# Optimization experiments

Measured on AMD Instinct MI355X. Metric: run time of the kernel, lower is better.

The kernel has to match this reference:

```python
import jax, jax.numpy as jnp
import numpy as np

A = 81          # agents / zones (9x9 grid)
DMAX = 5        # max neighborhood size (self + 4-neighbors)
NGLOB = 48      # global obs block width
HID = 128
B = 16384
LN_EPS = 1e-12  # tf.contrib.layers.layer_norm epsilon
BN_EPS = 1e-3   # tf.contrib.layers.batch_norm epsilon
NEG = -1e30


def _grid_adjacency():
    side = 9
    idx = np.zeros((A, DMAX), np.int32)
    mask = np.zeros((A, DMAX), bool)
    for i in range(A):
        r, c = divmod(i, side)
        nb = [i]
        for dr, dc in ((-1, 0), (1, 0), (0, -1), (0, 1)):
            rr, cc = r + dr, c + dc
            if 0 <= rr < side and 0 <= cc < side:
                nb.append(rr * side + cc)
        idx[i, :len(nb)] = nb
        mask[i, :len(nb)] = True
    return jnp.asarray(idx), jnp.asarray(mask)


def setup_inputs() -> dict:
    key = jax.random.key(0)
    ks = jax.random.split(key, 8)
    neigh_idx, neigh_mask = _grid_adjacency()
    in_dim = 2 * DMAX + NGLOB  # padded local obs width (58)
    s = 0.05
    return {
        "obs": jax.random.normal(ks[0], (B, 210), jnp.float32),
        "neigh_idx": neigh_idx,
        "neigh_mask": neigh_mask,
        "W1": jax.random.normal(ks[1], (A, in_dim, HID), jnp.float32) * s,
        "b1": jnp.zeros((A, HID), jnp.float32),
        "ln1_g": jnp.ones((A, HID), jnp.float32),
        "ln1_b": jnp.zeros((A, HID), jnp.float32),
        "bn1_b": jnp.zeros((A, HID), jnp.float32),
        "W2": jax.random.normal(ks[2], (A, HID, HID), jnp.float32) * s,
        "b2": jnp.zeros((A, HID), jnp.float32),
        "ln2_g": jnp.ones((A, HID), jnp.float32),
        "ln2_b": jnp.zeros((A, HID), jnp.float32),
        "bn2_b": jnp.zeros((A, HID), jnp.float32),
        "Wout": jax.random.normal(ks[3], (A, HID, DMAX), jnp.float32) * s,
        "bout": jnp.zeros((A, DMAX), jnp.float32),
    }


def _layer_norm(x, g, b):
    mu = jnp.mean(x, axis=-1, keepdims=True)
    var = jnp.mean(jnp.square(x - mu), axis=-1, keepdims=True)
    return (x - mu) * jax.lax.rsqrt(var + LN_EPS) * g[:, None, :] + b[:, None, :]


def _batch_norm(x, beta):
    # training-mode batch norm over the batch axis (axis=1), center only (scale=False)
    mu = jnp.mean(x, axis=1, keepdims=True)
    var = jnp.mean(jnp.square(x - mu), axis=1, keepdims=True)
    return (x - mu) * jax.lax.rsqrt(var + BN_EPS) + beta[:, None, :]


def reference(obs, neigh_idx, neigh_mask, W1, b1, ln1_g, ln1_b, bn1_b,
              W2, b2, ln2_g, ln2_b, bn2_b, Wout, bout):
    m = neigh_mask[:, None, :].astype(obs.dtype)          # [A,1,DMAX]
    g1 = obs[:, NGLOB + neigh_idx].transpose(1, 0, 2)      # [A,B,DMAX] zone block 1
    g2 = obs[:, NGLOB + 81 + neigh_idx].transpose(1, 0, 2)  # [A,B,DMAX] zone block 2
    glob = jnp.broadcast_to(obs[None, :, :NGLOB], (A, obs.shape[0], NGLOB))
    x = jnp.concatenate([g1 * m, g2 * m, glob], axis=-1)   # [A,B,58] (padded slots zeroed)

    h = jnp.einsum('abi,aio->abo', x, W1) + b1[:, None, :]
    h = jax.nn.relu(_batch_norm(_layer_norm(h, ln1_g, ln1_b), bn1_b))
    h = jnp.einsum('abi,aio->abo', h, W2) + b2[:, None, :]
    h = jax.nn.relu(_batch_norm(_layer_norm(h, ln2_g, ln2_b), bn2_b))

    logits = jnp.einsum('abi,aid->abd', h, Wout) + bout[:, None, :]  # [A,B,DMAX]
    logits = jnp.where(neigh_mask[:, None, :], logits, NEG)
    p = jax.nn.softmax(logits, axis=-1) * m                # masked softmax over valid neighbors

    oh = jax.nn.one_hot(neigh_idx, A, dtype=p.dtype)       # [A,DMAX,81] scatter map
    out = jnp.einsum('abd,adn->abn', p, oh)                # scatter into fixed 81-vector
    return out.transpose(1, 0, 2)                          # [B,A,81]
```

## Files before the change

### kernel.cpp

```cpp
#include <hip/hip_runtime.h>
#include <stdint.h>
#include <stddef.h>

#define N_AG 81

typedef __bf16 bf16x8 __attribute__((ext_vector_type(8)));
typedef float f32x4 __attribute__((ext_vector_type(4)));
typedef uint32_t u32v4 __attribute__((ext_vector_type(4)));
typedef uint32_t u32v2 __attribute__((ext_vector_type(2)));

#define PB 0
#define PG 128
#define PBT 256

#define SWZ(row, off) ((uint32_t)(off) ^ (((uint32_t)(row) & 7u) << 4))

__device__ __forceinline__ unsigned short b2u(__bf16 h) {
  return __builtin_bit_cast(unsigned short, h);
}

__device__ __forceinline__ f32x4 f4z() { f32x4 v; v[0]=0.f; v[1]=0.f; v[2]=0.f; v[3]=0.f; return v; }

__device__ __forceinline__ bf16x8 ld_frag(const uint8_t* p) {
  u32v4 v = *(const u32v4*)p;
  return __builtin_bit_cast(bf16x8, v);
}

__device__ __forceinline__ f32x4 mfma16(bf16x8 a, bf16x8 b, f32x4 c) {
  return __builtin_amdgcn_mfma_f32_16x16x32_bf16(a, b, c, 0, 0, 0);
}

__device__ __forceinline__ uint8_t* yslot(float* out, int b, int a) {
  size_t base = (size_t)b * 26244 + (size_t)a * 324;
  uint32_t pad = (uint32_t)(64 - (base & 63)) & 63u;
  return (uint8_t*)out + base + pad;
}

__device__ __forceinline__ float wave16_sum(float v) {
  v += __builtin_bit_cast(float, __builtin_amdgcn_update_dpp(0, __builtin_bit_cast(int, v), 0xB1, 0xF, 0xF, true));
  v += __builtin_bit_cast(float, __builtin_amdgcn_update_dpp(0, __builtin_bit_cast(int, v), 0x4E, 0xF, 0xF, true));
  v += __builtin_bit_cast(float, __builtin_amdgcn_update_dpp(0, __builtin_bit_cast(int, v), 0x141, 0xF, 0xF, true));
  v += __builtin_bit_cast(float, __builtin_amdgcn_update_dpp(0, __builtin_bit_cast(int, v), 0x140, 0xF, 0xF, true));
  return v;
}

__device__ __forceinline__ bf16x8 mk_frag(const unsigned short (&us)[8]) {
  u32v4 pk;
  pk[0] = (uint32_t)us[0] | ((uint32_t)us[1] << 16);
  pk[1] = (uint32_t)us[2] | ((uint32_t)us[3] << 16);
  pk[2] = (uint32_t)us[4] | ((uint32_t)us[5] << 16);
  pk[3] = (uint32_t)us[6] | ((uint32_t)us[7] << 16);
  return __builtin_bit_cast(bf16x8, pk);
}

__device__ __forceinline__ bf16x8 bn_frag(u32v4 yv, const f32x4 (&cf)[4]) {
  bf16x8 r;
  #pragma unroll
  for (int j = 0; j < 8; ++j) {
    uint32_t us = (j & 1) ? (yv[j >> 1] >> 16) : (yv[j >> 1] & 0xffffu);
    float f = __builtin_bit_cast(float, us << 16);
    float h = fmaf(f, cf[j >> 1][(j & 1) * 2], cf[j >> 1][(j & 1) * 2 + 1]);
    r[j] = (__bf16)fmaxf(h, 0.f);
  }
  return r;
}

__device__ __forceinline__ void bias_ln(f32x4 (&acc)[8][2], const float* s_par, int g) {
  #pragma unroll
  for (int nf = 0; nf < 2; ++nf) {
    float s = 0.f, qs = 0.f;
    #pragma unroll
    for (int mf = 0; mf < 8; ++mf) {
      #pragma unroll
      for (int rg = 0; rg < 4; ++rg) {
        float tv = acc[mf][nf][rg] + s_par[PB + 16 * mf + 4 * g + rg];
        acc[mf][nf][rg] = tv;
        s += tv;
        qs = fmaf(tv, tv, qs);
      }
    }
    s += __shfl_xor(s, 16);  s += __shfl_xor(s, 32);
    qs += __shfl_xor(qs, 16); qs += __shfl_xor(qs, 32);
    float mu = s * (1.f / 128.f);
    float var = qs * (1.f / 128.f) - mu * mu;
    float rstd = rsqrtf(var + 1e-12f);
    #pragma unroll
    for (int mf = 0; mf < 8; ++mf) {
      #pragma unroll
      for (int rg = 0; rg < 4; ++rg) {
        int o = 16 * mf + 4 * g + rg;
        acc[mf][nf][rg] = (acc[mf][nf][rg] - mu) * rstd * s_par[PG + o] + s_par[PBT + o];
      }
    }
  }
}

__device__ __forceinline__ void stats_lds(const f32x4 (&acc)[8][2],
                                          float (&s_red)[2][4][128],
                                          int wv, int g, int q) {
  #pragma unroll
  for (int mf = 0; mf < 8; ++mf) {
    #pragma unroll
    for (int rg = 0; rg < 4; ++rg) {
      float a0v = acc[mf][0][rg], a1v = acc[mf][1][rg];
      float s = a0v + a1v;
      float qq = fmaf(a0v, a0v, a1v * a1v);
      s = wave16_sum(s);
      qq = wave16_sum(qq);
      if (q == 0) {
        int o = 16 * mf + 4 * g + rg;
        s_red[0][wv][o] += s;
        s_red[1][wv][o] += qq;
      }
    }
  }
}

__device__ __forceinline__ void pack_lds(const f32x4 (&acc)[8][2], uint8_t* s_y,
                                         int wv, int g, int q) {
  #pragma unroll
  for (int nf = 0; nf < 2; ++nf) {
    uint32_t row = 32 * wv + 16 * nf + q;
    #pragma unroll
    for (int mf = 0; mf < 8; ++mf) {
      u32v2 pk;
      pk[0] = (uint32_t)b2u((__bf16)acc[mf][nf][0]) | ((uint32_t)b2u((__bf16)acc[mf][nf][1]) << 16);
      pk[1] = (uint32_t)b2u((__bf16)acc[mf][nf][2]) | ((uint32_t)b2u((__bf16)acc[mf][nf][3]) << 16);
      *(u32v2*)(s_y + row * 256 + SWZ(row, 32 * mf + 8 * g)) = pk;
    }
  }
}

__device__ __forceinline__ void burst_out(const uint8_t* s_y, float* out, int tile, int a, int t) {
  const int row = t >> 1, half = t & 1;
  uint8_t* sp = yslot(out, tile * 128 + row, a) + half * 128;
  #pragma unroll
  for (int j = 0; j < 8; ++j) {
    u32v4 v = *(const u32v4*)(s_y + row * 256 + SWZ(row, half * 128 + 16 * j));
    *(u32v4*)(sp + 16 * j) = v;
  }
}

__device__ __forceinline__ void burst_in(uint8_t* s_y, float* out, int tile, int a, int t) {
  const int row = t >> 1, half = t & 1;
  const uint8_t* sp = yslot(out, tile * 128 + row, a) + half * 128;
  #pragma unroll
  for (int j = 0; j < 8; ++j) {
    u32v4 v = *(const u32v4*)(sp + 16 * j);
    *(u32v4*)(s_y + row * 256 + SWZ(row, half * 128 + 16 * j)) = v;
  }
}

__global__ void prep_w1(const float* __restrict__ W1, uint8_t* __restrict__ w1img) {
  const int a = blockIdx.x, t = threadIdx.x;
  for (int i = t; i < 128 * 64; i += 256) {
    int o = i & 127, kk = i >> 7;
    float v;
    if (kk < 48)      v = W1[((size_t)a * 58 + (10 + kk)) * 128 + o];
    else if (kk < 58) v = W1[((size_t)a * 58 + (kk - 48)) * 128 + o];
    else              v = 0.f;
    uint32_t cb = 2u * kk;
    uint32_t phys = o * 128 + (((cb & ~15u) ^ (((uint32_t)o & 7u) << 4)) | (cb & 15u));
    *(unsigned short*)(w1img + (size_t)a * 16384 + phys) = b2u((__bf16)v);
  }
}

__global__ void prep_w2wo(const float* __restrict__ W2, const float* __restrict__ Wout,
                          uint8_t* __restrict__ w2img, uint8_t* __restrict__ woimg) {
  const int a = blockIdx.x, t = threadIdx.x;
  for (int i = t; i < 128 * 128; i += 256) {
    int o = i & 127, kk = i >> 7;
    float v = W2[((size_t)a * 128 + kk) * 128 + o];
    uint32_t cb = 2u * kk;
    uint32_t phys = o * 256 + (((cb & ~15u) ^ (((uint32_t)o & 7u) << 4)) | (cb & 15u));
    *(unsigned short*)(w2img + (size_t)a * 32768 + phys) = b2u((__bf16)v);
  }
  for (int i = t; i < 16 * 128; i += 256) {
    int k = i & 127, d = i >> 7;
    float v = (d < 5) ? Wout[((size_t)a * 128 + k) * 5 + d] : 0.f;
    uint32_t cb = 2u * k;
    uint32_t phys = d * 256 + (((cb & ~15u) ^ (((uint32_t)d & 7u) << 4)) | (cb & 15u));
    *(unsigned short*)(woimg + (size_t)a * 4096 + phys) = b2u((__bf16)v);
  }
}

__global__ void prep_obs(const float* __restrict__ obs, uint8_t* __restrict__ globimg) {
  const int row = blockIdx.x * 256 + threadIdx.x;
  if (row >= 16384) return;
  const float* orow = obs + (size_t)row * 210;
  uint8_t* dst = globimg + (size_t)row * 96;
  #pragma unroll
  for (int c = 0; c < 6; ++c) {
    u32v4 pk;
    #pragma unroll
    for (int e = 0; e < 4; ++e) {
      pk[e] = (uint32_t)b2u((__bf16)orow[8 * c + 2 * e]) |
              ((uint32_t)b2u((__bf16)orow[8 * c + 2 * e + 1]) << 16);
    }
    *(u32v4*)(dst + 16 * c) = pk;
  }
}

__global__ void prep_zimgT(const float* __restrict__ obs, unsigned short* __restrict__ zimgT) {
  __shared__ unsigned short lt[128][164];
  const int t = threadIdx.x;
  const int b0 = blockIdx.x * 128;
  for (int i = t; i < 128 * 162; i += 256) {
    int br = i / 162, n = i - 162 * br;
    lt[br][n] = b2u((__bf16)obs[(size_t)(b0 + br) * 210 + 48 + n]);
  }
  __syncthreads();
  for (int i = t; i < 162 * 128; i += 256) {
    int n = i >> 7, br = i & 127;
    zimgT[(size_t)n * 16384 + b0 + br] = lt[br][n];
  }
}

__global__ void reduce_bn(const float* __restrict__ S, const float* __restrict__ Q,
                          const float* __restrict__ beta, float2* __restrict__ bn) {
  const int a = blockIdx.x, k = threadIdx.x;
  float mu = S[a * 128 + k] * (1.f / 16384.f);
  float var = Q[a * 128 + k] * (1.f / 16384.f) - mu * mu;
  float rs = rsqrtf(var + 1e-3f);
  bn[a * 128 + k] = make_float2(rs, beta[a * 128 + k] - mu * rs);
}

__launch_bounds__(256, 2)
__global__ void pass1_kernel(const int* __restrict__ nidx,
                             const float* __restrict__ b1, const float* __restrict__ ln1g,
                             const float* __restrict__ ln1b,
                             const uint8_t* __restrict__ w1img,
                             const uint8_t* __restrict__ globimg,
                             const unsigned short* __restrict__ zimgT,
                             float* __restrict__ statS, float* __restrict__ statQ,
                             float* __restrict__ out) {
  __shared__ __align__(16) uint8_t s_w1[16384];
  __shared__ __align__(16) uint8_t s_y[32768];
  __shared__ float s_par[384];
  __shared__ float s_red[2][4][128];

  const int t = threadIdx.x;
  const int wv = t >> 6, l = t & 63, g = l >> 4, q = l & 15;
  const int a = blockIdx.x >> 5;
  const int sub = blockIdx.x & 31;

  const int r9 = a / 9, c9 = a - 9 * r9;
  const int deg = 1 + (r9 > 0) + (r9 < 8) + (c9 > 0) + (c9 < 8);
  int nid[5];
  #pragma unroll
  for (int d = 0; d < 5; ++d) nid[d] = __builtin_amdgcn_readfirstlane(nidx[a * 5 + d]);

  const uint8_t* w1src = w1img + (size_t)a * 16384;
  #pragma unroll
  for (int i = 0; i < 4; ++i) ((u32v4*)s_w1)[t + 256 * i] = ((const u32v4*)w1src)[t + 256 * i];
  if (t < 128) {
    s_par[PB + t] = b1[a * 128 + t];
    s_par[PG + t] = ln1g[a * 128 + t];
    s_par[PBT + t] = ln1b[a * 128 + t];
  }
  #pragma unroll
  for (int i = 0; i < 4; ++i) ((float*)s_red)[t + 256 * i] = 0.f;
  __syncthreads();

  for (int tt = 0; tt < 4; ++tt) {
    const int tile = sub * 4 + tt;

    bf16x8 bfr[2][2];
    #pragma unroll
    for (int ks = 0; ks < 2; ++ks) {
      #pragma unroll
      for (int nf = 0; nf < 2; ++nf) {
        const int brow = tile * 128 + 32 * wv + 16 * nf + q;
        if (ks == 1 && g >= 2) {
          unsigned short us[8];
          if (g == 2) {
            #pragma unroll
            for (int e = 0; e < 5; ++e)
              us[e] = (e < deg) ? zimgT[(size_t)nid[e] * 16384 + brow] : (unsigned short)0;
            #pragma unroll
            for (int e = 0; e < 3; ++e)
              us[5 + e] = (e < deg) ? zimgT[(size_t)(81 + nid[e]) * 16384 + brow] : (unsigned short)0;
          } else {
            us[0] = (3 < deg) ? zimgT[(size_t)(81 + nid[3]) * 16384 + brow] : (unsigned short)0;
            us[1] = (4 < deg) ? zimgT[(size_t)(81 + nid[4]) * 16384 + brow] : (unsigned short)0;
            #pragma unroll
            for (int e = 2; e < 8; ++e) us[e] = 0;
          }
          bfr[ks][nf] = mk_frag(us);
        } else {
          bfr[ks][nf] = *(const bf16x8*)(globimg + (size_t)brow * 96 + (32 * ks + 8 * g) * 2);
        }
      }
    }

    f32x4 acc[8][2];
    #pragma unroll
    for (int mf = 0; mf < 8; ++mf) { acc[mf][0] = f4z(); acc[mf][1] = f4z(); }
    #pragma unroll
    for (int ks = 0; ks < 2; ++ks) {
      #pragma unroll
      for (int mf = 0; mf < 8; ++mf) {
        uint32_t r = 16 * mf + q;
        uint32_t cb = ((uint32_t)(64 * ks + 16 * g)) ^ ((r & 7u) << 4);
        bf16x8 af = ld_frag(s_w1 + r * 128 + cb);
        acc[mf][0] = mfma16(af, bfr[ks][0], acc[mf][0]);
        acc[mf][1] = mfma16(af, bfr[ks][1], acc[mf][1]);
      }
    }

    bias_ln(acc, s_par, g);
    stats_lds(acc, s_red, wv, g, q);
    pack_lds(acc, s_y, wv, g, q);
    __syncthreads();
    burst_out(s_y, out, tile, a, t);
    __syncthreads();
  }

  if (t < 128) {
    float S = s_red[0][0][t] + s_red[0][1][t] + s_red[0][2][t] + s_red[0][3][t];
    float Q = s_red[1][0][t] + s_red[1][1][t] + s_red[1][2][t] + s_red[1][3][t];
    atomicAdd(statS + a * 128 + t, S);
    atomicAdd(statQ + a * 128 + t, Q);
  }
}

__launch_bounds__(256, 2)
__global__ void pass2_kernel(const float* __restrict__ b2, const float* __restrict__ ln2g,
                             const float* __restrict__ ln2b,
                             const uint8_t* __restrict__ w2img,
                             const float2* __restrict__ bn1,
                             float* __restrict__ statS, float* __restrict__ statQ,
                             float* __restrict__ out) {
  __shared__ __align__(16) uint8_t s_w2[32768];
  __shared__ __align__(16) uint8_t s_y[32768];
  __shared__ float s_par[384];
  __shared__ __align__(16) float2 s_bnc[128];
  __shared__ float s_red[2][4][128];

  const int t = threadIdx.x;
  const int wv = t >> 6, l = t & 63, g = l >> 4, q = l & 15;
  const int a = blockIdx.x >> 5;
  const int sub = blockIdx.x & 31;

  const uint8_t* w2src = w2img + (size_t)a * 32768;
  #pragma unroll
  for (int i = 0; i < 8; ++i) ((u32v4*)s_w2)[t + 256 * i] = ((const u32v4*)w2src)[t + 256 * i];
  if (t < 128) {
    s_par[PB + t] = b2[a * 128 + t];
    s_par[PG + t] = ln2g[a * 128 + t];
    s_par[PBT + t] = ln2b[a * 128 + t];
    s_bnc[t] = bn1[a * 128 + t];
  }
  #pragma unroll
  for (int i = 0; i < 4; ++i) ((float*)s_red)[t + 256 * i] = 0.f;
  __syncthreads();

  for (int tt = 0; tt < 4; ++tt) {
    const int tile = sub * 4 + tt;

    burst_in(s_y, out, tile, a, t);
    __syncthreads();

    f32x4 acc[8][2];
    #pragma unroll
    for (int mf = 0; mf < 8; ++mf) { acc[mf][0] = f4z(); acc[mf][1] = f4z(); }

    #pragma unroll
    for (int ks2 = 0; ks2 < 4; ++ks2) {
      const int k0 = 32 * ks2 + 8 * g;
      f32x4 cf[4];
      #pragma unroll
      for (int i = 0; i < 4; ++i)
        cf[i] = *(const f32x4*)((const uint8_t*)s_bnc + k0 * 8 + 16 * i);
      bf16x8 bfr[2];
      #pragma unroll
      for (int nf = 0; nf < 2; ++nf) {
        uint32_t row = 32 * wv + 16 * nf + q;
        u32v4 yv = *(const u32v4*)(s_y + row * 256 + SWZ(row, 64 * ks2 + 16 * g));
        bfr[nf] = bn_frag(yv, cf);
      }
      #pragma unroll
      for (int mf = 0; mf < 8; ++mf) {
        uint32_t r = 16 * mf + q;
        uint32_t cb = ((uint32_t)(64 * ks2 + 16 * g)) ^ ((r & 7u) << 4);
        bf16x8 af = ld_frag(s_w2 + r * 256 + cb);
        acc[mf][0] = mfma16(af, bfr[0], acc[mf][0]);
        acc[mf][1] = mfma16(af, bfr[1], acc[mf][1]);
      }
    }

    bias_ln(acc, s_par, g);
    stats_lds(acc, s_red, wv, g, q);
    __syncthreads();
    pack_lds(acc, s_y, wv, g, q);
    __syncthreads();
    burst_out(s_y, out, tile, a, t);
    __syncthreads();
  }

  if (t < 128) {
    float S = s_red[0][0][t] + s_red[0][1][t] + s_red[0][2][t] + s_red[0][3][t];
    float Q = s_red[1][0][t] + s_red[1][1][t] + s_red[1][2][t] + s_red[1][3][t];
    atomicAdd(statS + a * 128 + t, S);
    atomicAdd(statQ + a * 128 + t, Q);
  }
}

__launch_bounds__(256, 3)
__global__ void pass3_kernel(const int* __restrict__ nidx, const float* __restrict__ boutp,
                             const uint8_t* __restrict__ woimg,
                             const float2* __restrict__ bn2,
                             float* __restrict__ out) {
  __shared__ __align__(16) uint8_t s_buf[43008];
  __shared__ __align__(16) uint8_t s_wo[4096];
  __shared__ __align__(16) float2 s_bnc[128];
  __shared__ float s_bout[16];

  uint8_t* s_y = s_buf;
  float* s_out = (float*)s_buf;

  const int t = threadIdx.x;
  const int wv = t >> 6, l = t & 63, g = l >> 4, q = l & 15;
  const int a = blockIdx.x >> 5;
  const int sub = blockIdx.x & 31;

  const int r9 = a / 9, c9 = a - 9 * r9;
  const int deg = 1 + (r9 > 0) + (r9 < 8) + (c9 > 0) + (c9 < 8);
  int nid[5];
  #pragma unroll
  for (int d = 0; d < 5; ++d) nid[d] = __builtin_amdgcn_readfirstlane(nidx[a * 5 + d]);

  ((u32v4*)s_wo)[t] = ((const u32v4*)(woimg + (size_t)a * 4096))[t];
  if (t < 128) s_bnc[t] = bn2[a * 128 + t];
  if (t < 16) s_bout[t] = (t < 5) ? boutp[a * 5 + t] : 0.f;
  __syncthreads();

  bf16x8 afr[4];
  #pragma unroll
  for (int ks2 = 0; ks2 < 4; ++ks2) {
    uint32_t cb = ((uint32_t)(64 * ks2 + 16 * g)) ^ (((uint32_t)q & 7u) << 4);
    afr[ks2] = ld_frag(s_wo + q * 256 + cb);
  }

  for (int tt = 0; tt < 4; ++tt) {
    const int tile = sub * 4 + tt;

    burst_in(s_y, out, tile, a, t);
    __syncthreads();

    f32x4 accd[2];
    accd[0] = f4z(); accd[1] = f4z();

    #pragma unroll
    for (int ks2 = 0; ks2 < 4; ++ks2) {
      const int k0 = 32 * ks2 + 8 * g;
      f32x4 cf[4];
      #pragma unroll
      for (int i = 0; i < 4; ++i)
        cf[i] = *(const f32x4*)((const uint8_t*)s_bnc + k0 * 8 + 16 * i);
      #pragma unroll
      for (int nf = 0; nf < 2; ++nf) {
        uint32_t row = 32 * wv + 16 * nf + q;
        u32v4 yv = *(const u32v4*)(s_y + row * 256 + SWZ(row, 64 * ks2 + 16 * g));
        accd[nf] = mfma16(afr[ks2], bn_frag(yv, cf), accd[nf]);
      }
    }

    #pragma unroll
    for (int nf = 0; nf < 2; ++nf) {
      #pragma unroll
      for (int rg = 0; rg < 4; ++rg) accd[nf][rg] += s_bout[4 * g + rg];
    }
    float d4[2];
    d4[0] = __shfl_xor(accd[0][0], 16);
    d4[1] = __shfl_xor(accd[1][0], 16);

    float p[2][5];
    #pragma unroll
    for (int nf = 0; nf < 2; ++nf) {
      float v[5] = {accd[nf][0], accd[nf][1], accd[nf][2], accd[nf][3], d4[nf]};
      float mx = v[0];
      #pragma unroll
      for (int d = 1; d < 5; ++d)
        if (d < deg) mx = fmaxf(mx, v[d]);
      float den = 0.f;
      #pragma unroll
      for (int d = 0; d < 5; ++d) {
        float e = (d < deg) ? __expf(v[d] - mx) : 0.f;
        p[nf][d] = e;
        den += e;
      }
      float inv = 1.f / den;
      #pragma unroll
      for (int d = 0; d < 5; ++d) p[nf][d] *= inv;
    }

    float p5[5];
    #pragma unroll
    for (int d = 0; d < 5; ++d) {
      float pr = __shfl_xor(p[1][d], 32);
      p5[d] = (g == 0) ? p[0][d] : pr;
    }

    __syncthreads();
    #pragma unroll
    for (int i = 0; i < 11; ++i) {
      int idx = t + 256 * i;
      if (idx < 2688) {
        u32v4 z; z[0] = 0u; z[1] = 0u; z[2] = 0u; z[3] = 0u;
        ((u32v4*)s_out)[idx] = z;
      }
    }
    __syncthreads();
    if (g == 0 || g == 2) {
      const int row = 32 * wv + ((g == 2) ? 16 : 0) + q;
      #pragma unroll
      for (int d = 0; d < 5; ++d)
        if (d < deg) s_out[row * 84 + nid[d]] = p5[d];
    }
    __syncthreads();
    const size_t obase = (size_t)(tile * 128) * 6561 + (size_t)a * 81;
    for (int i = t; i < 128 * 81; i += 256) {
      int r = i / 81;
      int n = i - r * 81;
      out[obase + (size_t)r * 6561 + n] = s_out[r * 84 + n];
    }
    __syncthreads();
  }
}

extern "C" void kernel_launch(void* const* d_in, const int* in_sizes, int n_in,
                              void* d_out, int out_size, void* d_ws, size_t ws_size,
                              hipStream_t stream) {
  (void)in_sizes; (void)n_in; (void)out_size; (void)ws_size;
  const float* obs = (const float*)d_in[0];
  const int* nidx = (const int*)d_in[1];
  const float* W1 = (const float*)d_in[3];
  const float* b1 = (const float*)d_in[4];
  const float* ln1g = (const float*)d_in[5];
  const float* ln1b = (const float*)d_in[6];
  const float* bnb1 = (const float*)d_in[7];
  const float* W2 = (const float*)d_in[8];
  const float* b2 = (const float*)d_in[9];
  const float* ln2g = (const float*)d_in[10];
  const float* ln2b = (const float*)d_in[11];
  const float* bnb2 = (const float*)d_in[12];
  const float* Wout = (const float*)d_in[13];
  const float* bout = (const float*)d_in[14];
  float* out = (float*)d_out;
  uint8_t* ws = (uint8_t*)d_ws;

  uint8_t* w1img   = ws;
  uint8_t* globimg = ws + 1327104;
  uint8_t* regionA = ws + 2899968;
  unsigned short* zimgT = (unsigned short*)regionA;
  uint8_t* w2img = regionA;
  uint8_t* woimg = regionA + 2654208;
  float* statS = (float*)(ws + 8208384);
  float* statQ = (float*)(ws + 8249856);
  float2* bn1 = (float2*)(ws + 8291328);
  float2* bn2 = (float2*)(ws + 8374272);

  prep_w1<<<N_AG, 256, 0, stream>>>(W1, w1img);
  prep_obs<<<64, 256, 0, stream>>>(obs, globimg);
  prep_zimgT<<<128, 256, 0, stream>>>(obs, zimgT);
  hipMemsetAsync(statS, 0, 2 * 41472, stream);

  pass1_kernel<<<N_AG * 32, 256, 0, stream>>>(nidx, b1, ln1g, ln1b, w1img, globimg, zimgT,
                                              statS, statQ, out);
  reduce_bn<<<N_AG, 128, 0, stream>>>(statS, statQ, bnb1, bn1);

  prep_w2wo<<<N_AG, 256, 0, stream>>>(W2, Wout, w2img, woimg);
  hipMemsetAsync(statS, 0, 2 * 41472, stream);

  pass2_kernel<<<N_AG * 32, 256, 0, stream>>>(b2, ln2g, ln2b, w2img, bn1,
                                              statS, statQ, out);
  reduce_bn<<<N_AG, 128, 0, stream>>>(statS, statQ, bnb2, bn2);

  pass3_kernel<<<N_AG * 32, 256, 0, stream>>>(nidx, bout, woimg, bn2, out);
}
```

Before: 777.8 us.

## Use 512-thread blocks with one 16-row N-fragment per wave across passes

All three pass kernels move from 256 to 512 threads per block. Each of the 8 waves now owns 16 batch rows instead of 32, which halves the per-thread accumulator registers and lets more waves hide latency. Pass3 replaces the block-wide zero/scatter/copy of the output tile with per-wave bands, removing two block barriers per tile. reduce_bn now zeroes the stat buffers itself, which drops one memset launch, at the cost of less per-wave reuse of each loaded weight fragment.

New measurement: 958.0 us. +23.2%, slower.

```diff
diff --git a/kernel.cpp b/kernel.cpp
--- a/kernel.cpp
+++ b/kernel.cpp
@@ -65,46 +65,42 @@
   return r;
 }
 
-__device__ __forceinline__ void bias_ln(f32x4 (&acc)[8][2], const float* s_par, int g) {
-  #pragma unroll
-  for (int nf = 0; nf < 2; ++nf) {
-    float s = 0.f, qs = 0.f;
-    #pragma unroll
-    for (int mf = 0; mf < 8; ++mf) {
-      #pragma unroll
-      for (int rg = 0; rg < 4; ++rg) {
-        float tv = acc[mf][nf][rg] + s_par[PB + 16 * mf + 4 * g + rg];
-        acc[mf][nf][rg] = tv;
-        s += tv;
-        qs = fmaf(tv, tv, qs);
-      }
-    }
-    s += __shfl_xor(s, 16);  s += __shfl_xor(s, 32);
-    qs += __shfl_xor(qs, 16); qs += __shfl_xor(qs, 32);
-    float mu = s * (1.f / 128.f);
-    float var = qs * (1.f / 128.f) - mu * mu;
-    float rstd = rsqrtf(var + 1e-12f);
-    #pragma unroll
-    for (int mf = 0; mf < 8; ++mf) {
-      #pragma unroll
-      for (int rg = 0; rg < 4; ++rg) {
-        int o = 16 * mf + 4 * g + rg;
-        acc[mf][nf][rg] = (acc[mf][nf][rg] - mu) * rstd * s_par[PG + o] + s_par[PBT + o];
-      }
-    }
-  }
-}
-
-__device__ __forceinline__ void stats_lds(const f32x4 (&acc)[8][2],
-                                          float (&s_red)[2][4][128],
-                                          int wv, int g, int q) {
+__device__ __forceinline__ void bias_ln1(f32x4 (&acc)[8], const float* s_par, int g) {
+  float s = 0.f, qs = 0.f;
   #pragma unroll
   for (int mf = 0; mf < 8; ++mf) {
     #pragma unroll
     for (int rg = 0; rg < 4; ++rg) {
-      float a0v = acc[mf][0][rg], a1v = acc[mf][1][rg];
-      float s = a0v + a1v;
-      float qq = fmaf(a0v, a0v, a1v * a1v);
+      float tv = acc[mf][rg] + s_par[PB + 16 * mf + 4 * g + rg];
+      acc[mf][rg] = tv;
+      s += tv;
+      qs = fmaf(tv, tv, qs);
+    }
+  }
+  s += __shfl_xor(s, 16);  s += __shfl_xor(s, 32);
+  qs += __shfl_xor(qs, 16); qs += __shfl_xor(qs, 32);
+  float mu = s * (1.f / 128.f);
+  float var = qs * (1.f / 128.f) - mu * mu;
+  float rstd = rsqrtf(var + 1e-12f);
+  #pragma unroll
+  for (int mf = 0; mf < 8; ++mf) {
+    #pragma unroll
+    for (int rg = 0; rg < 4; ++rg) {
+      int o = 16 * mf + 4 * g + rg;
+      acc[mf][rg] = (acc[mf][rg] - mu) * rstd * s_par[PG + o] + s_par[PBT + o];
+    }
+  }
+}
+
+__device__ __forceinline__ void stats_lds1(const f32x4 (&acc)[8],
+                                           float (&s_red)[2][8][128],
+                                           int wv, int g, int q) {
+  #pragma unroll
+  for (int mf = 0; mf < 8; ++mf) {
+    #pragma unroll
+    for (int rg = 0; rg < 4; ++rg) {
+      float s = acc[mf][rg];
+      float qq = s * s;
       s = wave16_sum(s);
       qq = wave16_sum(qq);
       if (q == 0) {
@@ -116,38 +112,35 @@
   }
 }
 
-__device__ __forceinline__ void pack_lds(const f32x4 (&acc)[8][2], uint8_t* s_y,
-                                         int wv, int g, int q) {
-  #pragma unroll
-  for (int nf = 0; nf < 2; ++nf) {
-    uint32_t row = 32 * wv + 16 * nf + q;
-    #pragma unroll
-    for (int mf = 0; mf < 8; ++mf) {
-      u32v2 pk;
-      pk[0] = (uint32_t)b2u((__bf16)acc[mf][nf][0]) | ((uint32_t)b2u((__bf16)acc[mf][nf][1]) << 16);
-      pk[1] = (uint32_t)b2u((__bf16)acc[mf][nf][2]) | ((uint32_t)b2u((__bf16)acc[mf][nf][3]) << 16);
-      *(u32v2*)(s_y + row * 256 + SWZ(row, 32 * mf + 8 * g)) = pk;
-    }
-  }
-}
-
-__device__ __forceinline__ void burst_out(const uint8_t* s_y, float* out, int tile, int a, int t) {
-  const int row = t >> 1, half = t & 1;
-  uint8_t* sp = yslot(out, tile * 128 + row, a) + half * 128;
-  #pragma unroll
-  for (int j = 0; j < 8; ++j) {
-    u32v4 v = *(const u32v4*)(s_y + row * 256 + SWZ(row, half * 128 + 16 * j));
+__device__ __forceinline__ void pack_lds1(const f32x4 (&acc)[8], uint8_t* s_y,
+                                          int wv, int g, int q) {
+  uint32_t row = 16 * wv + q;
+  #pragma unroll
+  for (int mf = 0; mf < 8; ++mf) {
+    u32v2 pk;
+    pk[0] = (uint32_t)b2u((__bf16)acc[mf][0]) | ((uint32_t)b2u((__bf16)acc[mf][1]) << 16);
+    pk[1] = (uint32_t)b2u((__bf16)acc[mf][2]) | ((uint32_t)b2u((__bf16)acc[mf][3]) << 16);
+    *(u32v2*)(s_y + row * 256 + SWZ(row, 32 * mf + 8 * g)) = pk;
+  }
+}
+
+__device__ __forceinline__ void burst_out512(const uint8_t* s_y, float* out, int tile, int a, int t) {
+  const int row = t >> 2, qt = t & 3;
+  uint8_t* sp = yslot(out, tile * 128 + row, a) + qt * 64;
+  #pragma unroll
+  for (int j = 0; j < 4; ++j) {
+    u32v4 v = *(const u32v4*)(s_y + row * 256 + SWZ(row, qt * 64 + 16 * j));
     *(u32v4*)(sp + 16 * j) = v;
   }
 }
 
-__device__ __forceinline__ void burst_in(uint8_t* s_y, float* out, int tile, int a, int t) {
-  const int row = t >> 1, half = t & 1;
-  const uint8_t* sp = yslot(out, tile * 128 + row, a) + half * 128;
-  #pragma unroll
-  for (int j = 0; j < 8; ++j) {
+__device__ __forceinline__ void burst_in512(uint8_t* s_y, float* out, int tile, int a, int t) {
+  const int row = t >> 2, qt = t & 3;
+  const uint8_t* sp = yslot(out, tile * 128 + row, a) + qt * 64;
+  #pragma unroll
+  for (int j = 0; j < 4; ++j) {
     u32v4 v = *(const u32v4*)(sp + 16 * j);
-    *(u32v4*)(s_y + row * 256 + SWZ(row, half * 128 + 16 * j)) = v;
+    *(u32v4*)(s_y + row * 256 + SWZ(row, qt * 64 + 16 * j)) = v;
   }
 }
 
@@ -216,16 +209,18 @@
   }
 }
 
-__global__ void reduce_bn(const float* __restrict__ S, const float* __restrict__ Q,
+__global__ void reduce_bn(float* __restrict__ S, float* __restrict__ Q,
                           const float* __restrict__ beta, float2* __restrict__ bn) {
   const int a = blockIdx.x, k = threadIdx.x;
   float mu = S[a * 128 + k] * (1.f / 16384.f);
   float var = Q[a * 128 + k] * (1.f / 16384.f) - mu * mu;
   float rs = rsqrtf(var + 1e-3f);
   bn[a * 128 + k] = make_float2(rs, beta[a * 128 + k] - mu * rs);
-}
-
-__launch_bounds__(256, 2)
+  S[a * 128 + k] = 0.f;
+  Q[a * 128 + k] = 0.f;
+}
+
+__launch_bounds__(512, 4)
 __global__ void pass1_kernel(const int* __restrict__ nidx,
                              const float* __restrict__ b1, const float* __restrict__ ln1g,
                              const float* __restrict__ ln1b,
@@ -237,7 +232,7 @@
   __shared__ __align__(16) uint8_t s_w1[16384];
   __shared__ __align__(16) uint8_t s_y[32768];
   __shared__ float s_par[384];
-  __shared__ float s_red[2][4][128];
+  __shared__ float s_red[2][8][128];
 
   const int t = threadIdx.x;
   const int wv = t >> 6, l = t & 63, g = l >> 4, q = l & 15;
@@ -252,50 +247,47 @@
 
   const uint8_t* w1src = w1img + (size_t)a * 16384;
   #pragma unroll
-  for (int i = 0; i < 4; ++i) ((u32v4*)s_w1)[t + 256 * i] = ((const u32v4*)w1src)[t + 256 * i];
+  for (int i = 0; i < 2; ++i) ((u32v4*)s_w1)[t + 512 * i] = ((const u32v4*)w1src)[t + 512 * i];
   if (t < 128) {
     s_par[PB + t] = b1[a * 128 + t];
     s_par[PG + t] = ln1g[a * 128 + t];
     s_par[PBT + t] = ln1b[a * 128 + t];
   }
   #pragma unroll
-  for (int i = 0; i < 4; ++i) ((float*)s_red)[t + 256 * i] = 0.f;
+  for (int i = 0; i < 4; ++i) ((float*)s_red)[t + 512 * i] = 0.f;
   __syncthreads();
 
   for (int tt = 0; tt < 4; ++tt) {
     const int tile = sub * 4 + tt;
-
-    bf16x8 bfr[2][2];
+    const int brow = tile * 128 + 16 * wv + q;
+
+    bf16x8 bfr[2];
     #pragma unroll
     for (int ks = 0; ks < 2; ++ks) {
-      #pragma unroll
-      for (int nf = 0; nf < 2; ++nf) {
-        const int brow = tile * 128 + 32 * wv + 16 * nf + q;
-        if (ks == 1 && g >= 2) {
-          unsigned short us[8];
-          if (g == 2) {
-            #pragma unroll
-            for (int e = 0; e < 5; ++e)
-              us[e] = (e < deg) ? zimgT[(size_t)nid[e] * 16384 + brow] : (unsigned short)0;
-            #pragma unroll
-            for (int e = 0; e < 3; ++e)
-              us[5 + e] = (e < deg) ? zimgT[(size_t)(81 + nid[e]) * 16384 + brow] : (unsigned short)0;
-          } else {
-            us[0] = (3 < deg) ? zimgT[(size_t)(81 + nid[3]) * 16384 + brow] : (unsigned short)0;
-            us[1] = (4 < deg) ? zimgT[(size_t)(81 + nid[4]) * 16384 + brow] : (unsigned short)0;
-            #pragma unroll
-            for (int e = 2; e < 8; ++e) us[e] = 0;
-          }
-          bfr[ks][nf] = mk_frag(us);
+      if (ks == 1 && g >= 2) {
+        unsigned short us[8];
+        if (g == 2) {
+          #pragma unroll
+          for (int e = 0; e < 5; ++e)
+            us[e] = (e < deg) ? zimgT[(size_t)nid[e] * 16384 + brow] : (unsigned short)0;
+          #pragma unroll
+          for (int e = 0; e < 3; ++e)
+            us[5 + e] = (e < deg) ? zimgT[(size_t)(81 + nid[e]) * 16384 + brow] : (unsigned short)0;
         } else {
-          bfr[ks][nf] = *(const bf16x8*)(globimg + (size_t)brow * 96 + (32 * ks + 8 * g) * 2);
+          us[0] = (3 < deg) ? zimgT[(size_t)(81 + nid[3]) * 16384 + brow] : (unsigned short)0;
+          us[1] = (4 < deg) ? zimgT[(size_t)(81 + nid[4]) * 16384 + brow] : (unsigned short)0;
+          #pragma unroll
+          for (int e = 2; e < 8; ++e) us[e] = 0;
         }
-      }
-    }
-
-    f32x4 acc[8][2];
-    #pragma unroll
-    for (int mf = 0; mf < 8; ++mf) { acc[mf][0] = f4z(); acc[mf][1] = f4z(); }
+        bfr[ks] = mk_frag(us);
+      } else {
+        bfr[ks] = *(const bf16x8*)(globimg + (size_t)brow * 96 + (32 * ks + 8 * g) * 2);
+      }
+    }
+
+    f32x4 acc[8];
+    #pragma unroll
+    for (int mf = 0; mf < 8; ++mf) acc[mf] = f4z();
     #pragma unroll
     for (int ks = 0; ks < 2; ++ks) {
       #pragma unroll
@@ -303,28 +295,28 @@
         uint32_t r = 16 * mf + q;
         uint32_t cb = ((uint32_t)(64 * ks + 16 * g)) ^ ((r & 7u) << 4);
         bf16x8 af = ld_frag(s_w1 + r * 128 + cb);
-        acc[mf][0] = mfma16(af, bfr[ks][0], acc[mf][0]);
-        acc[mf][1] = mfma16(af, bfr[ks][1], acc[mf][1]);
-      }
-    }
-
-    bias_ln(acc, s_par, g);
-    stats_lds(acc, s_red, wv, g, q);
-    pack_lds(acc, s_y, wv, g, q);
-    __syncthreads();
-    burst_out(s_y, out, tile, a, t);
+        acc[mf] = mfma16(af, bfr[ks], acc[mf]);
+      }
+    }
+
+    bias_ln1(acc, s_par, g);
+    stats_lds1(acc, s_red, wv, g, q);
+    pack_lds1(acc, s_y, wv, g, q);
+    __syncthreads();
+    burst_out512(s_y, out, tile, a, t);
     __syncthreads();
   }
 
   if (t < 128) {
-    float S = s_red[0][0][t] + s_red[0][1][t] + s_red[0][2][t] + s_red[0][3][t];
-    float Q = s_red[1][0][t] + s_red[1][1][t] + s_red[1][2][t] + s_red[1][3][t];
+    float S = 0.f, Q = 0.f;
+    #pragma unroll
+    for (int w = 0; w < 8; ++w) { S += s_red[0][w][t]; Q += s_red[1][w][t]; }
     atomicAdd(statS + a * 128 + t, S);
     atomicAdd(statQ + a * 128 + t, Q);
   }
 }
 
-__launch_bounds__(256, 2)
+__launch_bounds__(512, 4)
 __global__ void pass2_kernel(const float* __restrict__ b2, const float* __restrict__ ln2g,
                              const float* __restrict__ ln2b,
                              const uint8_t* __restrict__ w2img,
@@ -335,7 +327,7 @@
   __shared__ __align__(16) uint8_t s_y[32768];
   __shared__ float s_par[384];
   __shared__ __align__(16) float2 s_bnc[128];
-  __shared__ float s_red[2][4][128];
+  __shared__ float s_red[2][8][128];
 
   const int t = threadIdx.x;
   const int wv = t >> 6, l = t & 63, g = l >> 4, q = l & 15;
@@ -344,7 +336,7 @@
 
   const uint8_t* w2src = w2img + (size_t)a * 32768;
   #pragma unroll
-  for (int i = 0; i < 8; ++i) ((u32v4*)s_w2)[t + 256 * i] = ((const u32v4*)w2src)[t + 256 * i];
+  for (int i = 0; i < 4; ++i) ((u32v4*)s_w2)[t + 512 * i] = ((const u32v4*)w2src)[t + 512 * i];
   if (t < 128) {
     s_par[PB + t] = b2[a * 128 + t];
     s_par[PG + t] = ln2g[a * 128 + t];
@@ -352,18 +344,19 @@
     s_bnc[t] = bn1[a * 128 + t];
   }
   #pragma unroll
-  for (int i = 0; i < 4; ++i) ((float*)s_red)[t + 256 * i] = 0.f;
+  for (int i = 0; i < 4; ++i) ((float*)s_red)[t + 512 * i] = 0.f;
   __syncthreads();
 
   for (int tt = 0; tt < 4; ++tt) {
     const int tile = sub * 4 + tt;
-
-    burst_in(s_y, out, tile, a, t);
-    __syncthreads();
-
-    f32x4 acc[8][2];
-    #pragma unroll
-    for (int mf = 0; mf < 8; ++mf) { acc[mf][0] = f4z(); acc[mf][1] = f4z(); }
+    const uint32_t row = 16 * wv + q;
+
+    burst_in512(s_y, out, tile, a, t);
+    __syncthreads();
+
+    f32x4 acc[8];
+    #pragma unroll
+    for (int mf = 0; mf < 8; ++mf) acc[mf] = f4z();
 
     #pragma unroll
     for (int ks2 = 0; ks2 < 4; ++ks2) {
@@ -372,41 +365,35 @@
       #pragma unroll
       for (int i = 0; i < 4; ++i)
         cf[i] = *(const f32x4*)((const uint8_t*)s_bnc + k0 * 8 + 16 * i);
-      bf16x8 bfr[2];
-      #pragma unroll
-      for (int nf = 0; nf < 2; ++nf) {
-        uint32_t row = 32 * wv + 16 * nf + q;
-        u32v4 yv = *(const u32v4*)(s_y + row * 256 + SWZ(row, 64 * ks2 + 16 * g));
-        bfr[nf] = bn_frag(yv, cf);
-      }
+      u32v4 yv = *(const u32v4*)(s_y + row * 256 + SWZ(row, 64 * ks2 + 16 * g));
+      bf16x8 bfr = bn_frag(yv, cf);
       #pragma unroll
       for (int mf = 0; mf < 8; ++mf) {
         uint32_t r = 16 * mf + q;
         uint32_t cb = ((uint32_t)(64 * ks2 + 16 * g)) ^ ((r & 7u) << 4);
         bf16x8 af = ld_frag(s_w2 + r * 256 + cb);
-        acc[mf][0] = mfma16(af, bfr[0], acc[mf][0]);
-        acc[mf][1] = mfma16(af, bfr[1], acc[mf][1]);
-      }
-    }
-
-    bias_ln(acc, s_par, g);
-    stats_lds(acc, s_red, wv, g, q);
-    __syncthreads();
-    pack_lds(acc, s_y, wv, g, q);
-    __syncthreads();
-    burst_out(s_y, out, tile, a, t);
+        acc[mf] = mfma16(af, bfr, acc[mf]);
+      }
+    }
+
+    bias_ln1(acc, s_par, g);
+    stats_lds1(acc, s_red, wv, g, q);
+    pack_lds1(acc, s_y, wv, g, q);
+    __syncthreads();
+    burst_out512(s_y, out, tile, a, t);
     __syncthreads();
   }
 
   if (t < 128) {
-    float S = s_red[0][0][t] + s_red[0][1][t] + s_red[0][2][t] + s_red[0][3][t];
-    float Q = s_red[1][0][t] + s_red[1][1][t] + s_red[1][2][t] + s_red[1][3][t];
+    float S = 0.f, Q = 0.f;
+    #pragma unroll
+    for (int w = 0; w < 8; ++w) { S += s_red[0][w][t]; Q += s_red[1][w][t]; }
     atomicAdd(statS + a * 128 + t, S);
     atomicAdd(statQ + a * 128 + t, Q);
   }
 }
 
-__launch_bounds__(256, 3)
+__launch_bounds__(512, 6)
 __global__ void pass3_kernel(const int* __restrict__ nidx, const float* __restrict__ boutp,
                              const uint8_t* __restrict__ woimg,
                              const float2* __restrict__ bn2,
@@ -430,7 +417,7 @@
   #pragma unroll
   for (int d = 0; d < 5; ++d) nid[d] = __builtin_amdgcn_readfirstlane(nidx[a * 5 + d]);
 
-  ((u32v4*)s_wo)[t] = ((const u32v4*)(woimg + (size_t)a * 4096))[t];
+  if (t < 256) ((u32v4*)s_wo)[t] = ((const u32v4*)(woimg + (size_t)a * 4096))[t];
   if (t < 128) s_bnc[t] = bn2[a * 128 + t];
   if (t < 16) s_bout[t] = (t < 5) ? boutp[a * 5 + t] : 0.f;
   __syncthreads();
@@ -444,13 +431,12 @@
 
   for (int tt = 0; tt < 4; ++tt) {
     const int tile = sub * 4 + tt;
-
-    burst_in(s_y, out, tile, a, t);
-    __syncthreads();
-
-    f32x4 accd[2];
-    accd[0] = f4z(); accd[1] = f4z();
-
+    const uint32_t row = 16 * wv + q;
+
+    burst_in512(s_y, out, tile, a, t);
+    __syncthreads();
+
+    f32x4 accd = f4z();
     #pragma unroll
     for (int ks2 = 0; ks2 < 4; ++ks2) {
       const int k0 = 32 * ks2 + 8 * g;
@@ -458,27 +444,17 @@
       #pragma unroll
       for (int i = 0; i < 4; ++i)
         cf[i] = *(const f32x4*)((const uint8_t*)s_bnc + k0 * 8 + 16 * i);
-      #pragma unroll
-      for (int nf = 0; nf < 2; ++nf) {
-        uint32_t row = 32 * wv + 16 * nf + q;
-        u32v4 yv = *(const u32v4*)(s_y + row * 256 + SWZ(row, 64 * ks2 + 16 * g));
-        accd[nf] = mfma16(afr[ks2], bn_frag(yv, cf), accd[nf]);
-      }
-    }
-
-    #pragma unroll
-    for (int nf = 0; nf < 2; ++nf) {
-      #pragma unroll
-      for (int rg = 0; rg < 4; ++rg) accd[nf][rg] += s_bout[4 * g + rg];
-    }
-    float d4[2];
-    d4[0] = __shfl_xor(accd[0][0], 16);
-    d4[1] = __shfl_xor(accd[1][0], 16);
-
-    float p[2][5];
-    #pragma unroll
-    for (int nf = 0; nf < 2; ++nf) {
-      float v[5] = {accd[nf][0], accd[nf][1], accd[nf][2], accd[nf][3], d4[nf]};
+      u32v4 yv = *(const u32v4*)(s_y + row * 256 + SWZ(row, 64 * ks2 + 16 * g));
+      accd = mfma16(afr[ks2], bn_frag(yv, cf), accd);
+    }
+
+    #pragma unroll
+    for (int rg = 0; rg < 4; ++rg) accd[rg] += s_bout[4 * g + rg];
+    float d4 = __shfl_xor(accd[0], 16);
+
+    float p[5];
+    {
+      float v[5] = {accd[0], accd[1], accd[2], accd[3], d4};
       float mx = v[0];
       #pragma unroll
       for (int d = 1; d < 5; ++d)
@@ -487,44 +463,36 @@
       #pragma unroll
       for (int d = 0; d < 5; ++d) {
         float e = (d < deg) ? __expf(v[d] - mx) : 0.f;
-        p[nf][d] = e;
+        p[d] = e;
         den += e;
       }
       float inv = 1.f / den;
       #pragma unroll
-      for (int d = 0; d < 5; ++d) p[nf][d] *= inv;
-    }
-
-    float p5[5];
-    #pragma unroll
-    for (int d = 0; d < 5; ++d) {
-      float pr = __shfl_xor(p[1][d], 32);
-      p5[d] = (g == 0) ? p[0][d] : pr;
-    }
-
-    __syncthreads();
-    #pragma unroll
-    for (int i = 0; i < 11; ++i) {
-      int idx = t + 256 * i;
-      if (idx < 2688) {
+      for (int d = 0; d < 5; ++d) p[d] *= inv;
+    }
+
+    __syncthreads();
+
+    {
+      uint8_t* band = (uint8_t*)s_out + (size_t)wv * 5376;
+      for (int i = l; i < 336; i += 64) {
         u32v4 z; z[0] = 0u; z[1] = 0u; z[2] = 0u; z[3] = 0u;
-        ((u32v4*)s_out)[idx] = z;
-      }
-    }
-    __syncthreads();
-    if (g == 0 || g == 2) {
-      const int row = 32 * wv + ((g == 2) ? 16 : 0) + q;
-      #pragma unroll
-      for (int d = 0; d < 5; ++d)
-        if (d < deg) s_out[row * 84 + nid[d]] = p5[d];
-    }
-    __syncthreads();
-    const size_t obase = (size_t)(tile * 128) * 6561 + (size_t)a * 81;
-    for (int i = t; i < 128 * 81; i += 256) {
-      int r = i / 81;
-      int n = i - r * 81;
-      out[obase + (size_t)r * 6561 + n] = s_out[r * 84 + n];
-    }
+        *(u32v4*)(band + (size_t)i * 16) = z;
+      }
+      if (g == 0) {
+        #pragma unroll
+        for (int d = 0; d < 5; ++d)
+          if (d < deg) s_out[(16 * wv + q) * 84 + nid[d]] = p[d];
+      }
+      const size_t obase = (size_t)(tile * 128) * 6561 + (size_t)a * 81;
+      for (int i = l; i < 16 * 81; i += 64) {
+        int rr = i / 81;
+        int n = i - rr * 81;
+        int orow = 16 * wv + rr;
+        out[obase + (size_t)orow * 6561 + n] = s_out[orow * 84 + n];
+      }
+    }
+
     __syncthreads();
   }
 }
@@ -566,16 +534,15 @@
   prep_zimgT<<<128, 256, 0, stream>>>(obs, zimgT);
   hipMemsetAsync(statS, 0, 2 * 41472, stream);
 
-  pass1_kernel<<<N_AG * 32, 256, 0, stream>>>(nidx, b1, ln1g, ln1b, w1img, globimg, zimgT,
+  pass1_kernel<<<N_AG * 32, 512, 0, stream>>>(nidx, b1, ln1g, ln1b, w1img, globimg, zimgT,
                                               statS, statQ, out);
   reduce_bn<<<N_AG, 128, 0, stream>>>(statS, statQ, bnb1, bn1);
 
   prep_w2wo<<<N_AG, 256, 0, stream>>>(W2, Wout, w2img, woimg);
-  hipMemsetAsync(statS, 0, 2 * 41472, stream);
-
-  pass2_kernel<<<N_AG * 32, 256, 0, stream>>>(b2, ln2g, ln2b, w2img, bn1,
+
+  pass2_kernel<<<N_AG * 32, 512, 0, stream>>>(b2, ln2g, ln2b, w2img, bn1,
                                               statS, statQ, out);
   reduce_bn<<<N_AG, 128, 0, stream>>>(statS, statQ, bnb2, bn2);
 
-  pass3_kernel<<<N_AG * 32, 256, 0, stream>>>(nidx, bout, woimg, bn2, out);
-}
+  pass3_kernel<<<N_AG * 32, 512, 0, stream>>>(nidx, bout, woimg, bn2, out);
+}
```
